# Kernel tuning notes

Hardware: AMD Instinct MI355X
Metric: run time of the kernel (lower is better)

The kernel has to match this reference:

```python
import jax, jax.numpy as jnp
import numpy as np

B, S, H, NH = 4, 2048, 1024, 16
D = H // NH  # head width = 64
SCALE = 1.0 / np.sqrt(np.float32(H))  # NOTE: module scales by rsqrt(hidden_size), not head_width
EPS = 1e-5


def setup_inputs() -> dict:
    key = jax.random.key(0)
    ks = jax.random.split(key, 12)
    def lin(k):
        kw, kb = jax.random.split(k)
        return (jax.random.normal(kw, (H, H), jnp.float32) * 0.02,
                jax.random.normal(kb, (H,), jnp.float32) * 0.02)
    Wq, bq = lin(ks[0]); Wk, bk = lin(ks[1]); Wv, bv = lin(ks[2]); Wm, bm = lin(ks[3])
    q = jax.random.normal(ks[4], (B, S, H), jnp.float32)
    k = jax.random.normal(ks[5], (B, S, H), jnp.float32)
    v = jax.random.normal(ks[6], (B, S, H), jnp.float32)
    # causal mask: True positions are masked with -inf (matches masked_fill semantics)
    mask = jnp.broadcast_to(jnp.triu(jnp.ones((S, S), bool), k=1), (B, S, S))
    gamma = jnp.ones((H,), jnp.float32)
    beta = jnp.zeros((H,), jnp.float32)
    return {"q": q, "k": k, "v": v, "mask": mask,
            "Wq": Wq, "bq": bq, "Wk": Wk, "bk": bk, "Wv": Wv, "bv": bv,
            "Wm": Wm, "bm": bm, "gamma": gamma, "beta": beta}


def layer_norm(x, gamma, beta):
    mu = jnp.mean(x, axis=-1, keepdims=True)
    var = jnp.mean(jnp.square(x - mu), axis=-1, keepdims=True)
    return (x - mu) * jax.lax.rsqrt(var + EPS) * gamma + beta


def reference(q, k, v, mask, Wq, bq, Wk, bk, Wv, bv, Wm, bm, gamma, beta):
    residual = q
    # projections, split into heads: [B, NH, S, D]
    qh = (q @ Wq.T + bq).reshape(B, S, NH, D).transpose(0, 2, 1, 3)
    kh = (k @ Wk.T + bk).reshape(B, S, NH, D).transpose(0, 2, 1, 3)
    vh = (v @ Wv.T + bv).reshape(B, S, NH, D).transpose(0, 2, 1, 3)
    scores = jnp.einsum('bhsd,bhtd->bhst', qh, kh) * SCALE
    scores = jnp.where(mask[:, None, :, :], -jnp.inf, scores)
    attn = jax.nn.softmax(scores, axis=-1)  # dropout is identity (p=0 / eval)
    ctx = jnp.einsum('bhst,bhtd->bhsd', attn, vh)
    ctx = ctx.transpose(0, 2, 1, 3).reshape(B, S, H)
    out = ctx @ Wm.T + bm
    out = layer_norm(out + residual, gamma, beta)
    return out, attn
```

## Files before the change

kernel.cpp:

```cpp
#include <hip/hip_runtime.h>
#include <hip/hip_bf16.h>

#define S_LEN   2048
#define NHEAD   16
#define HID     1024
#define HDIM    64
#define ATT_SCALE 0.03125f
#define LN_EPS  1e-5f
#define EXP_C1  0.04508422002778011f
#define EXP_C2  (-11.541560327111707f)

using bf16x8 = __attribute__((ext_vector_type(8))) short;
using f32x4  = __attribute__((ext_vector_type(4))) float;
typedef unsigned short u16;

__device__ __forceinline__ u16 f2b(float f) {
  union { float f; unsigned u; } v; v.f = f;
  unsigned r = v.u + 0x7fffu + ((v.u >> 16) & 1u);
  return (u16)(r >> 16);
}

__device__ __forceinline__ float fexp2(float x) {
  return __builtin_amdgcn_exp2f(x);
}

__device__ __forceinline__ unsigned cvtpk(float a, float b) {
  unsigned r;
  asm("v_cvt_pk_bf16_f32 %0, %1, %2" : "=v"(r) : "v"(a), "v"(b));
  return r;
}

__device__ __forceinline__ f32x4 mfma16(bf16x8 a, bf16x8 b, f32x4 c) {
  return __builtin_amdgcn_mfma_f32_16x16x32_bf16(a, b, c, 0, 0, 0);
}

__device__ __forceinline__ void gld_lds16(const u16* g, void* l) {
  __builtin_amdgcn_global_load_lds(
      (const __attribute__((address_space(1))) void*)g,
      (__attribute__((address_space(3))) void*)l, 16, 0, 0);
}

__global__ __launch_bounds__(256) void cvt_w4(
    const float* __restrict__ s0, const float* __restrict__ s1,
    const float* __restrict__ s2, const float* __restrict__ s3,
    u16* __restrict__ d0, u16* __restrict__ d1,
    u16* __restrict__ d2, u16* __restrict__ d3)
{
  int i = blockIdx.x * 256 + threadIdx.x;
  int stride = gridDim.x * 256;
  for (; i < 1048576; i += stride) {
    int seg = i >> 18, off = i & 262143;
    const float* s = seg == 0 ? s0 : seg == 1 ? s1 : seg == 2 ? s2 : s3;
    u16*         d = seg == 0 ? d0 : seg == 1 ? d1 : seg == 2 ? d2 : d3;
    float4 vv = ((const float4*)s)[off];
    ushort4 o;
    o.x = f2b(vv.x); o.y = f2b(vv.y); o.z = f2b(vv.z); o.w = f2b(vv.w);
    ((ushort4*)d)[off] = o;
  }
}

__global__ __launch_bounds__(256) void cvt_x3(
    const float* __restrict__ s0, const float* __restrict__ s1,
    const float* __restrict__ s2,
    u16* __restrict__ d0, u16* __restrict__ d1, u16* __restrict__ d2)
{
  int i = blockIdx.x * 256 + threadIdx.x;
  int stride = gridDim.x * 256;
  for (; i < 6291456; i += stride) {
    int seg = i >> 21, off = i & 2097151;
    const float* s = seg == 0 ? s0 : seg == 1 ? s1 : s2;
    u16*         d = seg == 0 ? d0 : seg == 1 ? d1 : d2;
    float4 vv = ((const float4*)s)[off];
    ushort4 o;
    o.x = f2b(vv.x); o.y = f2b(vv.y); o.z = f2b(vv.z); o.w = f2b(vv.w);
    ((ushort4*)d)[off] = o;
  }
}

__global__ __launch_bounds__(256) void qkv_gemm(
    const u16* __restrict__ xq, const u16* __restrict__ xk,
    const u16* __restrict__ xv,
    const u16* __restrict__ Wq, const u16* __restrict__ Wk,
    const u16* __restrict__ Wv,
    const float* __restrict__ bq, const float* __restrict__ bk,
    const float* __restrict__ bv,
    u16* __restrict__ qo, u16* __restrict__ ko, u16* __restrict__ vo,
    float* __restrict__ fill)
{
  const int t = threadIdx.x;

  if (blockIdx.y >= 192) {
    int u = ((int)blockIdx.y - 192) * 8 + (int)blockIdx.x;
    int bh = u & 63, tmp = u >> 6, qtb = tmp >> 3, rg = tmp & 7;
    int w4 = (15 - qtb) * 32;
    f32x4* base = (f32x4*)(fill + ((long)bh * 2048 + qtb * 128 + rg * 16) * 2048
                                + (qtb + 1) * 128);
    f32x4 z = { 0.f, 0.f, 0.f, 0.f };
    for (int r = 0; r < 16; ++r) {
      f32x4* rp = base + (long)r * 512;
      for (int cc = t; cc < w4; cc += 256) rp[cc] = z;
    }
    return;
  }

  const int yg = blockIdx.y;
  const int op = yg >> 6;
  const u16*   A    = op == 0 ? xq : op == 1 ? xk : xv;
  const u16*   W    = op == 0 ? Wq : op == 1 ? Wk : Wv;
  const float* bias = op == 0 ? bq : op == 1 ? bk : bv;
  u16*         out  = op == 0 ? qo : op == 1 ? ko : vo;

  __shared__ __align__(16) u16 As[128 * 64];
  __shared__ __align__(16) u16 Bs[128 * 64];
  const int m0 = (yg & 63) * 128, n0 = blockIdx.x * 128;
  const int w = t >> 6, lane = t & 63, g = lane >> 4, c = lane & 15;
  const int wr = w >> 1, wc = w & 1;

  f32x4 acc[4][4] = {};

  for (int k0 = 0; k0 < 1024; k0 += 64) {
    __syncthreads();
#pragma unroll
    for (int it = 0; it < 4; ++it) {
      int chunk = it * 256 + t;
      int row = chunk >> 3, cf = (chunk & 7) * 8;
      gld_lds16(&A[(long)(m0 + row) * 1024 + k0 + cf], &As[(it * 256 + (t & ~63)) * 8]);
      gld_lds16(&W[(long)(n0 + row) * 1024 + k0 + cf], &Bs[(it * 256 + (t & ~63)) * 8]);
    }
    __syncthreads();
#pragma unroll
    for (int kk = 0; kk < 2; ++kk) {
      bf16x8 am[4], bn[4];
#pragma unroll
      for (int m = 0; m < 4; ++m)
        am[m] = *(const bf16x8*)(&As[(wr * 64 + m * 16 + c) * 64 + kk * 32 + g * 8]);
#pragma unroll
      for (int n = 0; n < 4; ++n)
        bn[n] = *(const bf16x8*)(&Bs[(wc * 64 + n * 16 + c) * 64 + kk * 32 + g * 8]);
#pragma unroll
      for (int m = 0; m < 4; ++m)
#pragma unroll
        for (int n = 0; n < 4; ++n)
          acc[m][n] = mfma16(am[m], bn[n], acc[m][n]);
    }
  }

#pragma unroll
  for (int m = 0; m < 4; ++m)
#pragma unroll
    for (int n = 0; n < 4; ++n)
#pragma unroll
      for (int r = 0; r < 4; ++r) {
        int grow = m0 + wr * 64 + m * 16 + g * 4 + r;
        int gcol = n0 + wc * 64 + n * 16 + c;
        float v = acc[m][n][r] + bias[gcol];
        int b = grow >> 11, s = grow & 2047;
        int h = gcol >> 6, d = gcol & 63;
        out[(((long)(b * 16 + h) * 2048 + s) << 6) + d] = f2b(v);
      }
}

__global__ __launch_bounds__(256) void gemm_out(
    const u16* __restrict__ A, const u16* __restrict__ W,
    float* __restrict__ out_f)
{
  __shared__ __align__(16) u16 As[128 * 64];
  __shared__ __align__(16) u16 Bs[128 * 64];
  const int t = threadIdx.x;
  const int m0 = blockIdx.y * 128, n0 = blockIdx.x * 128;
  const int w = t >> 6, lane = t & 63, g = lane >> 4, c = lane & 15;
  const int wr = w >> 1, wc = w & 1;

  f32x4 acc[4][4] = {};

  for (int k0 = 0; k0 < 1024; k0 += 64) {
    __syncthreads();
#pragma unroll
    for (int it = 0; it < 4; ++it) {
      int chunk = it * 256 + t;
      int row = chunk >> 3, cf = (chunk & 7) * 8;
      gld_lds16(&A[(long)(m0 + row) * 1024 + k0 + cf], &As[(it * 256 + (t & ~63)) * 8]);
      gld_lds16(&W[(long)(n0 + row) * 1024 + k0 + cf], &Bs[(it * 256 + (t & ~63)) * 8]);
    }
    __syncthreads();
#pragma unroll
    for (int kk = 0; kk < 2; ++kk) {
      bf16x8 am[4], bn[4];
#pragma unroll
      for (int m = 0; m < 4; ++m)
        am[m] = *(const bf16x8*)(&As[(wr * 64 + m * 16 + c) * 64 + kk * 32 + g * 8]);
#pragma unroll
      for (int n = 0; n < 4; ++n)
        bn[n] = *(const bf16x8*)(&Bs[(wc * 64 + n * 16 + c) * 64 + kk * 32 + g * 8]);
#pragma unroll
      for (int m = 0; m < 4; ++m)
#pragma unroll
        for (int n = 0; n < 4; ++n)
          acc[m][n] = mfma16(am[m], bn[n], acc[m][n]);
    }
  }

#pragma unroll
  for (int m = 0; m < 4; ++m)
#pragma unroll
    for (int n = 0; n < 4; ++n)
#pragma unroll
      for (int r = 0; r < 4; ++r) {
        int grow = m0 + wr * 64 + m * 16 + g * 4 + r;
        int gcol = n0 + wc * 64 + n * 16 + c;
        out_f[(long)grow * 1024 + gcol] = acc[m][n][r];
      }
}

__global__ __launch_bounds__(256) void transpose_v(const u16* __restrict__ vh,
                                                   u16* __restrict__ vt) {
  __shared__ __align__(16) u16 tile[64 * 72];
  const int t = threadIdx.x;
  const u16* src = vh + ((long)blockIdx.y * 2048 + blockIdx.x * 64) * 64;
#pragma unroll
  for (int it = 0; it < 2; ++it) {
    int chunk = it * 256 + t;
    int s = chunk >> 3, d0 = (chunk & 7) * 8;
    *(int4*)(&tile[s * 72 + d0]) = *(const int4*)(&src[s * 64 + d0]);
  }
  __syncthreads();
  u16* dst = vt + (long)blockIdx.y * 64 * 2048 + blockIdx.x * 64;
#pragma unroll
  for (int it = 0; it < 2; ++it) {
    int chunk = it * 256 + t;
    int d = chunk >> 3, s0 = (chunk & 7) * 8;
    __attribute__((ext_vector_type(8))) unsigned short v;
#pragma unroll
    for (int x = 0; x < 8; ++x) v[x] = tile[(s0 + x) * 72 + d];
    *(decltype(v)*)(&dst[(long)d * 2048 + s0]) = v;
  }
}

__global__ __launch_bounds__(512, 4) void attn_kernel(
    const u16* __restrict__ qh, const u16* __restrict__ kh,
    const u16* __restrict__ vt, u16* __restrict__ ctx,
    float* __restrict__ attn)
{
  __shared__ __align__(16) char lds[49152];
  const int t = threadIdx.x, w = t >> 6, lane = t & 63, g = lane >> 4, c = lane & 15;
  const int n = blockIdx.x;
  const int bh = (n & 7) * 8 + ((n >> 3) & 7);
  const int qtb = 15 - (n >> 6);
  const int q0 = qtb * 128;
  const int ktmax = qtb * 2 + 1;
  const long kvbase = (long)bh * 2048 * 64;

  bf16x8 qa[2];
  {
    const u16* qp = qh + kvbase + (long)(q0 + w * 16 + c) * 64 + g * 8;
    qa[0] = *(const bf16x8*)(qp);
    qa[1] = *(const bf16x8*)(qp + 32);
  }
  const int qpos = q0 + w * 16 + c;

  const int srow = t >> 3, sc8 = t & 7;
  const int ksoff = srow * 64 + ((sc8 ^ (srow & 7)) * 8);
  const u16* kbase = kh + kvbase;
  const u16* vbase = vt + (long)(bh * 64 + srow) * 2048 + ((sc8 ^ (srow & 7)) * 8);

  float lsum = 0.f;
  {
    gld_lds16(kbase + ksoff, lds + w * 1024);
    gld_lds16(kbase + 4096 + ksoff, lds + 8192 + w * 1024);
    for (int p = 0; p <= qtb; ++p) {
      const int kb = (p & 1) * 16384;
      if (p < qtb) {
        const int nb = ((p + 1) & 1) * 16384;
        gld_lds16(kbase + (long)(p + 1) * 8192 + ksoff, lds + nb + w * 1024);
        gld_lds16(kbase + (long)(p + 1) * 8192 + 4096 + ksoff, lds + nb + 8192 + w * 1024);
        asm volatile("s_waitcnt vmcnt(2)" ::: "memory");
      } else {
        asm volatile("s_waitcnt vmcnt(0)" ::: "memory");
      }
      __builtin_amdgcn_sched_barrier(0);
      __builtin_amdgcn_s_barrier();
      __builtin_amdgcn_sched_barrier(0);
      f32x4 sacc[8] = {};
      __builtin_amdgcn_s_setprio(1);
#pragma unroll
      for (int sub = 0; sub < 8; ++sub) {
        int row = sub * 16 + c;
#pragma unroll
        for (int kk = 0; kk < 2; ++kk) {
          bf16x8 av = *(const bf16x8*)(lds + kb + row * 128 + (((kk * 4 + g) ^ (c & 7)) << 4));
          sacc[sub] = mfma16(av, qa[kk], sacc[sub]);
        }
      }
      __builtin_amdgcn_s_setprio(0);
#pragma unroll
      for (int sub = 0; sub < 8; ++sub)
#pragma unroll
        for (int r = 0; r < 4; ++r) {
          int kpos = p * 128 + sub * 16 + g * 4 + r;
          float e = fexp2(fmaf(sacc[sub][r], EXP_C1, EXP_C2));
          lsum += (kpos > qpos) ? 0.f : e;
        }
      __builtin_amdgcn_sched_barrier(0);
      __builtin_amdgcn_s_barrier();
    }
  }
  lsum += __shfl_xor(lsum, 16, 64);
  lsum += __shfl_xor(lsum, 32, 64);
  const float ri = 1.f / lsum;

  char* const Ps = lds + 32768 + w * 2048;
  f32x4 oacc[4] = {};
  gld_lds16(kbase + ksoff, lds + w * 1024);
  gld_lds16(vbase, lds + 16384 + w * 1024);
  for (int kt = 0; kt <= ktmax; ++kt) {
    const int kb = (kt & 1) * 8192;
    if (kt < ktmax) {
      const int nb = ((kt + 1) & 1) * 8192;
      gld_lds16(kbase + (long)(kt + 1) * 4096 + ksoff, lds + nb + w * 1024);
      gld_lds16(vbase + (kt + 1) * 64, lds + 16384 + nb + w * 1024);
      if (kt == 0) { asm volatile("s_waitcnt vmcnt(2)" ::: "memory"); }
      else         { asm volatile("s_waitcnt vmcnt(6)" ::: "memory"); }
    } else {
      asm volatile("s_waitcnt vmcnt(4)" ::: "memory");
    }
    __builtin_amdgcn_sched_barrier(0);
    __builtin_amdgcn_s_barrier();
    __builtin_amdgcn_sched_barrier(0);
    f32x4 sacc[4] = {};
    __builtin_amdgcn_s_setprio(1);
#pragma unroll
    for (int sub = 0; sub < 4; ++sub) {
      int row = sub * 16 + c;
#pragma unroll
      for (int kk = 0; kk < 2; ++kk) {
        bf16x8 av = *(const bf16x8*)(lds + kb + row * 128 + (((kk * 4 + g) ^ (c & 7)) << 4));
        sacc[sub] = mfma16(av, qa[kk], sacc[sub]);
      }
    }
    __builtin_amdgcn_s_setprio(0);
#pragma unroll
    for (int sub = 0; sub < 4; ++sub) {
      float p[4];
#pragma unroll
      for (int r = 0; r < 4; ++r) {
        int kpos = kt * 64 + sub * 16 + g * 4 + r;
        float e = fexp2(fmaf(sacc[sub][r], EXP_C1, EXP_C2)) * ri;
        p[r] = (kpos > qpos) ? 0.f : e;
      }
      uint2 pk = { cvtpk(p[0], p[1]), cvtpk(p[2], p[3]) };
      int chunk = sub * 2 + (g >> 1);
      *(uint2*)(Ps + c * 128 + ((chunk ^ (c & 7)) << 4) + (g & 1) * 8) = pk;
    }
    {
      float* arow0 = attn + ((long)bh * 2048 + q0 + w * 16) * 2048 + kt * 64;
#pragma unroll
      for (int j = 0; j < 4; ++j) {
        int row = j * 4 + g;
        uint2 u = *(const uint2*)(Ps + row * 128 + (((c >> 1) ^ (row & 7)) << 4) + (c & 1) * 8);
        f32x4 pv;
        pv[0] = __uint_as_float((u.x & 0xffffu) << 16);
        pv[1] = __uint_as_float(u.x & 0xffff0000u);
        pv[2] = __uint_as_float((u.y & 0xffffu) << 16);
        pv[3] = __uint_as_float(u.y & 0xffff0000u);
        *(f32x4*)(arow0 + (long)row * 2048 + c * 4) = pv;
      }
    }
    __builtin_amdgcn_s_setprio(1);
#pragma unroll
    for (int kk = 0; kk < 2; ++kk) {
      bf16x8 pa = *(const bf16x8*)(Ps + c * 128 + (((kk * 4 + g) ^ (c & 7)) << 4));
#pragma unroll
      for (int db = 0; db < 4; ++db) {
        bf16x8 vb = *(const bf16x8*)(lds + 16384 + kb + (db * 16 + c) * 128 + (((kk * 4 + g) ^ (c & 7)) << 4));
        oacc[db] = mfma16(pa, vb, oacc[db]);
      }
    }
    __builtin_amdgcn_s_setprio(0);
    __builtin_amdgcn_sched_barrier(0);
    __builtin_amdgcn_s_barrier();
  }

  {
    int b = bh >> 4, h = bh & 15;
#pragma unroll
    for (int db = 0; db < 4; ++db)
#pragma unroll
      for (int r = 0; r < 4; ++r) {
        int s = q0 + w * 16 + g * 4 + r;
        ctx[(long)(b * 2048 + s) * 1024 + h * 64 + db * 16 + c] = f2b(oacc[db][r]);
      }
  }
}

__global__ __launch_bounds__(256) void ln_kernel(
    const float* __restrict__ y, const float* __restrict__ bm,
    const float* __restrict__ resid, const float* __restrict__ gamma,
    const float* __restrict__ beta, float* __restrict__ out)
{
  __shared__ float red[8];
  const long row = blockIdx.x;
  const int t = threadIdx.x, w = t >> 6, lane = t & 63;
  const float4* yp = (const float4*)(y + row * 1024);
  const float4* rp = (const float4*)(resid + row * 1024);
  float4 x = yp[t], rv = rp[t], bv = ((const float4*)bm)[t];
  x.x += rv.x + bv.x; x.y += rv.y + bv.y; x.z += rv.z + bv.z; x.w += rv.w + bv.w;

  float s1 = x.x + x.y + x.z + x.w;
#pragma unroll
  for (int o = 32; o; o >>= 1) s1 += __shfl_xor(s1, o, 64);
  if (!lane) red[w] = s1;
  __syncthreads();
  float mean = (red[0] + red[1] + red[2] + red[3]) * (1.f / 1024.f);

  float dx = x.x - mean, dy = x.y - mean, dz = x.z - mean, dw = x.w - mean;
  float s2 = dx * dx + dy * dy + dz * dz + dw * dw;
#pragma unroll
  for (int o = 32; o; o >>= 1) s2 += __shfl_xor(s2, o, 64);
  if (!lane) red[4 + w] = s2;
  __syncthreads();
  float var = (red[4] + red[5] + red[6] + red[7]) * (1.f / 1024.f);
  float rs = rsqrtf(var + LN_EPS);

  float4 gv = ((const float4*)gamma)[t], be = ((const float4*)beta)[t];
  float4 o4;
  o4.x = dx * rs * gv.x + be.x;
  o4.y = dy * rs * gv.y + be.y;
  o4.z = dz * rs * gv.z + be.z;
  o4.w = dw * rs * gv.w + be.w;
  ((float4*)(out + row * 1024))[t] = o4;
}

extern "C" void kernel_launch(void* const* d_in, const int* in_sizes, int n_in,
                              void* d_out, int out_size, void* d_ws, size_t ws_size,
                              hipStream_t stream) {
  const float* q     = (const float*)d_in[0];
  const float* k     = (const float*)d_in[1];
  const float* v     = (const float*)d_in[2];
  const float* Wq    = (const float*)d_in[4];
  const float* bq    = (const float*)d_in[5];
  const float* Wk    = (const float*)d_in[6];
  const float* bk    = (const float*)d_in[7];
  const float* Wv    = (const float*)d_in[8];
  const float* bv    = (const float*)d_in[9];
  const float* Wm    = (const float*)d_in[10];
  const float* bm    = (const float*)d_in[11];
  const float* gamma = (const float*)d_in[12];
  const float* beta  = (const float*)d_in[13];

  float* out  = (float*)d_out;
  float* attn = out + 8388608;

  char* ws = (char*)d_ws;
  u16* qh   = (u16*)(ws);
  u16* kh   = (u16*)(ws + 16777216);
  u16* vh   = (u16*)(ws + 33554432);
  u16* ctx  = (u16*)(ws + 33554432);
  u16* Wqb  = (u16*)(ws + 50331648);
  u16* Wkb  = Wqb + 1048576;
  u16* Wvb  = Wkb + 1048576;
  u16* Wmb  = Wvb + 1048576;
  u16* xq   = (u16*)(ws + 58720256);
  u16* vt   = (u16*)(ws + 58720256);
  u16* xk   = (u16*)(ws + 75497472);
  u16* xv   = (u16*)(ws + 92274688);
  float* y  = (float*)(ws + 75497472);

  dim3 blk(256);

  cvt_w4<<<1024, blk, 0, stream>>>(Wq, Wk, Wv, Wm, Wqb, Wkb, Wvb, Wmb);
  cvt_x3<<<2048, blk, 0, stream>>>(q, k, v, xq, xk, xv);

  qkv_gemm<<<dim3(8, 1152), blk, 0, stream>>>(
      xq, xk, xv, Wqb, Wkb, Wvb, bq, bk, bv, qh, kh, vh, attn);

  transpose_v<<<dim3(32, 64), blk, 0, stream>>>(vh, vt);

  attn_kernel<<<1024, 512, 0, stream>>>(qh, kh, vt, ctx, attn);

  gemm_out<<<dim3(8, 64), blk, 0, stream>>>(ctx, Wmb, y);

  ln_kernel<<<8192, blk, 0, stream>>>(y, bm, q, gamma, beta, out);
}
```

Baseline: 465.1 us.

## Double per-block query tile to 256 rows with triple-buffered K/V loads

Each attention block now handles 256 query rows (two 16-row groups per wave) instead of 128, so every K/V tile loaded into LDS is reused across twice as many queries and the grid halves to 512 blocks. K/V staging moves from double to triple buffering with adjusted vmcnt waits, and the per-iteration end barrier is removed. Block ordering is changed so the heavy and light causal tiles are interleaved for load balance. The cost is more LDS (64KB) and registers per block, which lowers occupancy and leaves fewer blocks to spread across CUs. Dropping the trailing barrier depends on the third buffer to keep the reused Ps and K/V regions free of read/write races.

```diff
diff --git a/kernel.cpp b/kernel.cpp
--- a/kernel.cpp
+++ b/kernel.cpp
@@ -241,38 +241,44 @@
     const u16* __restrict__ vt, u16* __restrict__ ctx,
     float* __restrict__ attn)
 {
-  __shared__ __align__(16) char lds[49152];
+  __shared__ __align__(16) char lds[65536];
   const int t = threadIdx.x, w = t >> 6, lane = t & 63, g = lane >> 4, c = lane & 15;
   const int n = blockIdx.x;
+  const int qtb = (n < 256) ? 7 - (n >> 6) : ((n - 256) >> 6);
   const int bh = (n & 7) * 8 + ((n >> 3) & 7);
-  const int qtb = 15 - (n >> 6);
-  const int q0 = qtb * 128;
-  const int ktmax = qtb * 2 + 1;
+  const int q0 = qtb * 256;
+  const int pmax  = qtb * 2 + 1;
+  const int ktmax = qtb * 4 + 3;
   const long kvbase = (long)bh * 2048 * 64;
 
-  bf16x8 qa[2];
+  bf16x8 qa[2][2];
+  int qpos[2];
+#pragma unroll
+  for (int h = 0; h < 2; ++h) {
+    const u16* qp = qh + kvbase + (long)(q0 + w * 32 + h * 16 + c) * 64 + g * 8;
+    qa[h][0] = *(const bf16x8*)(qp);
+    qa[h][1] = *(const bf16x8*)(qp + 32);
+    qpos[h] = q0 + w * 32 + h * 16 + c;
+  }
+
+  const int srow = t >> 3, sc8 = t & 7;
+  const int scol = (sc8 ^ (srow & 7)) * 8;
+  const u16* kbase = kh + kvbase;
+  const u16* vbase = vt + (long)(bh * 64 + srow) * 2048 + scol;
+
+  float lsum[2] = { 0.f, 0.f };
   {
-    const u16* qp = qh + kvbase + (long)(q0 + w * 16 + c) * 64 + g * 8;
-    qa[0] = *(const bf16x8*)(qp);
-    qa[1] = *(const bf16x8*)(qp + 32);
-  }
-  const int qpos = q0 + w * 16 + c;
-
-  const int srow = t >> 3, sc8 = t & 7;
-  const int ksoff = srow * 64 + ((sc8 ^ (srow & 7)) * 8);
-  const u16* kbase = kh + kvbase;
-  const u16* vbase = vt + (long)(bh * 64 + srow) * 2048 + ((sc8 ^ (srow & 7)) * 8);
-
-  float lsum = 0.f;
-  {
-    gld_lds16(kbase + ksoff, lds + w * 1024);
-    gld_lds16(kbase + 4096 + ksoff, lds + 8192 + w * 1024);
-    for (int p = 0; p <= qtb; ++p) {
-      const int kb = (p & 1) * 16384;
-      if (p < qtb) {
-        const int nb = ((p + 1) & 1) * 16384;
-        gld_lds16(kbase + (long)(p + 1) * 8192 + ksoff, lds + nb + w * 1024);
-        gld_lds16(kbase + (long)(p + 1) * 8192 + 4096 + ksoff, lds + nb + 8192 + w * 1024);
+#pragma unroll
+    for (int j = 0; j < 2; ++j)
+      gld_lds16(kbase + (j * 64 + srow) * 64 + scol, lds + j * 8192 + w * 1024);
+    for (int p = 0; p <= pmax; ++p) {
+      const int cur = (p % 3) * 16384;
+      if (p < pmax) {
+        const int nb = ((p + 1) % 3) * 16384;
+#pragma unroll
+        for (int j = 0; j < 2; ++j)
+          gld_lds16(kbase + ((long)(p + 1) * 128 + j * 64 + srow) * 64 + scol,
+                    lds + nb + j * 8192 + w * 1024);
         asm volatile("s_waitcnt vmcnt(2)" ::: "memory");
       } else {
         asm volatile("s_waitcnt vmcnt(0)" ::: "memory");
@@ -280,115 +286,126 @@
       __builtin_amdgcn_sched_barrier(0);
       __builtin_amdgcn_s_barrier();
       __builtin_amdgcn_sched_barrier(0);
-      f32x4 sacc[8] = {};
-      __builtin_amdgcn_s_setprio(1);
-#pragma unroll
-      for (int sub = 0; sub < 8; ++sub) {
-        int row = sub * 16 + c;
-#pragma unroll
-        for (int kk = 0; kk < 2; ++kk) {
-          bf16x8 av = *(const bf16x8*)(lds + kb + row * 128 + (((kk * 4 + g) ^ (c & 7)) << 4));
-          sacc[sub] = mfma16(av, qa[kk], sacc[sub]);
+#pragma unroll
+      for (int h = 0; h < 2; ++h) {
+        f32x4 sacc[8] = {};
+        __builtin_amdgcn_s_setprio(1);
+#pragma unroll
+        for (int sub = 0; sub < 8; ++sub) {
+          int row = sub * 16 + c;
+#pragma unroll
+          for (int kk = 0; kk < 2; ++kk) {
+            bf16x8 av = *(const bf16x8*)(lds + cur + row * 128 + (((kk * 4 + g) ^ (c & 7)) << 4));
+            sacc[sub] = mfma16(av, qa[h][kk], sacc[sub]);
+          }
         }
-      }
-      __builtin_amdgcn_s_setprio(0);
-#pragma unroll
-      for (int sub = 0; sub < 8; ++sub)
-#pragma unroll
-        for (int r = 0; r < 4; ++r) {
-          int kpos = p * 128 + sub * 16 + g * 4 + r;
-          float e = fexp2(fmaf(sacc[sub][r], EXP_C1, EXP_C2));
-          lsum += (kpos > qpos) ? 0.f : e;
-        }
-      __builtin_amdgcn_sched_barrier(0);
-      __builtin_amdgcn_s_barrier();
-    }
-  }
-  lsum += __shfl_xor(lsum, 16, 64);
-  lsum += __shfl_xor(lsum, 32, 64);
-  const float ri = 1.f / lsum;
-
-  char* const Ps = lds + 32768 + w * 2048;
-  f32x4 oacc[4] = {};
-  gld_lds16(kbase + ksoff, lds + w * 1024);
-  gld_lds16(vbase, lds + 16384 + w * 1024);
+        __builtin_amdgcn_s_setprio(0);
+#pragma unroll
+        for (int sub = 0; sub < 8; ++sub)
+#pragma unroll
+          for (int r = 0; r < 4; ++r) {
+            int kpos = p * 128 + sub * 16 + g * 4 + r;
+            float e = fexp2(fmaf(sacc[sub][r], EXP_C1, EXP_C2));
+            lsum[h] += (kpos > qpos[h]) ? 0.f : e;
+          }
+      }
+    }
+  }
+  float ri[2];
+#pragma unroll
+  for (int h = 0; h < 2; ++h) {
+    lsum[h] += __shfl_xor(lsum[h], 16, 64);
+    lsum[h] += __shfl_xor(lsum[h], 32, 64);
+    ri[h] = 1.f / lsum[h];
+  }
+  __builtin_amdgcn_sched_barrier(0);
+  __builtin_amdgcn_s_barrier();
+  __builtin_amdgcn_sched_barrier(0);
+
+  char* const Ps = lds + 49152 + w * 2048;
+  f32x4 oacc[2][4] = {};
+  gld_lds16(kbase + srow * 64 + scol, lds + w * 1024);
+  gld_lds16(vbase, lds + 24576 + w * 1024);
   for (int kt = 0; kt <= ktmax; ++kt) {
-    const int kb = (kt & 1) * 8192;
+    const int cur = (kt % 3) * 8192;
     if (kt < ktmax) {
-      const int nb = ((kt + 1) & 1) * 8192;
-      gld_lds16(kbase + (long)(kt + 1) * 4096 + ksoff, lds + nb + w * 1024);
-      gld_lds16(vbase + (kt + 1) * 64, lds + 16384 + nb + w * 1024);
+      const int nb = ((kt + 1) % 3) * 8192;
+      gld_lds16(kbase + (long)(kt + 1) * 4096 + srow * 64 + scol, lds + nb + w * 1024);
+      gld_lds16(vbase + (kt + 1) * 64, lds + 24576 + nb + w * 1024);
       if (kt == 0) { asm volatile("s_waitcnt vmcnt(2)" ::: "memory"); }
-      else         { asm volatile("s_waitcnt vmcnt(6)" ::: "memory"); }
+      else         { asm volatile("s_waitcnt vmcnt(10)" ::: "memory"); }
     } else {
-      asm volatile("s_waitcnt vmcnt(4)" ::: "memory");
+      asm volatile("s_waitcnt vmcnt(8)" ::: "memory");
     }
     __builtin_amdgcn_sched_barrier(0);
     __builtin_amdgcn_s_barrier();
     __builtin_amdgcn_sched_barrier(0);
-    f32x4 sacc[4] = {};
-    __builtin_amdgcn_s_setprio(1);
-#pragma unroll
-    for (int sub = 0; sub < 4; ++sub) {
-      int row = sub * 16 + c;
+#pragma unroll
+    for (int h = 0; h < 2; ++h) {
+      f32x4 sacc[4] = {};
+      __builtin_amdgcn_s_setprio(1);
+#pragma unroll
+      for (int sub = 0; sub < 4; ++sub) {
+        int row = sub * 16 + c;
+#pragma unroll
+        for (int kk = 0; kk < 2; ++kk) {
+          bf16x8 av = *(const bf16x8*)(lds + cur + row * 128 + (((kk * 4 + g) ^ (c & 7)) << 4));
+          sacc[sub] = mfma16(av, qa[h][kk], sacc[sub]);
+        }
+      }
+      __builtin_amdgcn_s_setprio(0);
+#pragma unroll
+      for (int sub = 0; sub < 4; ++sub) {
+        float p[4];
+#pragma unroll
+        for (int r = 0; r < 4; ++r) {
+          int kpos = kt * 64 + sub * 16 + g * 4 + r;
+          float e = fexp2(fmaf(sacc[sub][r], EXP_C1, EXP_C2)) * ri[h];
+          p[r] = (kpos > qpos[h]) ? 0.f : e;
+        }
+        uint2 pk = { cvtpk(p[0], p[1]), cvtpk(p[2], p[3]) };
+        int chunk = sub * 2 + (g >> 1);
+        *(uint2*)(Ps + c * 128 + ((chunk ^ (c & 7)) << 4) + (g & 1) * 8) = pk;
+      }
+      {
+        float* arow0 = attn + ((long)bh * 2048 + q0 + w * 32 + h * 16) * 2048 + kt * 64;
+#pragma unroll
+        for (int j = 0; j < 4; ++j) {
+          int row = j * 4 + g;
+          uint2 u = *(const uint2*)(Ps + row * 128 + (((c >> 1) ^ (row & 7)) << 4) + (c & 1) * 8);
+          f32x4 pv;
+          pv[0] = __uint_as_float((u.x & 0xffffu) << 16);
+          pv[1] = __uint_as_float(u.x & 0xffff0000u);
+          pv[2] = __uint_as_float((u.y & 0xffffu) << 16);
+          pv[3] = __uint_as_float(u.y & 0xffff0000u);
+          *(f32x4*)(arow0 + (long)row * 2048 + c * 4) = pv;
+        }
+      }
+      __builtin_amdgcn_s_setprio(1);
 #pragma unroll
       for (int kk = 0; kk < 2; ++kk) {
-        bf16x8 av = *(const bf16x8*)(lds + kb + row * 128 + (((kk * 4 + g) ^ (c & 7)) << 4));
-        sacc[sub] = mfma16(av, qa[kk], sacc[sub]);
-      }
-    }
-    __builtin_amdgcn_s_setprio(0);
-#pragma unroll
-    for (int sub = 0; sub < 4; ++sub) {
-      float p[4];
-#pragma unroll
-      for (int r = 0; r < 4; ++r) {
-        int kpos = kt * 64 + sub * 16 + g * 4 + r;
-        float e = fexp2(fmaf(sacc[sub][r], EXP_C1, EXP_C2)) * ri;
-        p[r] = (kpos > qpos) ? 0.f : e;
-      }
-      uint2 pk = { cvtpk(p[0], p[1]), cvtpk(p[2], p[3]) };
-      int chunk = sub * 2 + (g >> 1);
-      *(uint2*)(Ps + c * 128 + ((chunk ^ (c & 7)) << 4) + (g & 1) * 8) = pk;
-    }
-    {
-      float* arow0 = attn + ((long)bh * 2048 + q0 + w * 16) * 2048 + kt * 64;
-#pragma unroll
-      for (int j = 0; j < 4; ++j) {
-        int row = j * 4 + g;
-        uint2 u = *(const uint2*)(Ps + row * 128 + (((c >> 1) ^ (row & 7)) << 4) + (c & 1) * 8);
-        f32x4 pv;
-        pv[0] = __uint_as_float((u.x & 0xffffu) << 16);
-        pv[1] = __uint_as_float(u.x & 0xffff0000u);
-        pv[2] = __uint_as_float((u.y & 0xffffu) << 16);
-        pv[3] = __uint_as_float(u.y & 0xffff0000u);
-        *(f32x4*)(arow0 + (long)row * 2048 + c * 4) = pv;
-      }
-    }
-    __builtin_amdgcn_s_setprio(1);
-#pragma unroll
-    for (int kk = 0; kk < 2; ++kk) {
-      bf16x8 pa = *(const bf16x8*)(Ps + c * 128 + (((kk * 4 + g) ^ (c & 7)) << 4));
-#pragma unroll
-      for (int db = 0; db < 4; ++db) {
-        bf16x8 vb = *(const bf16x8*)(lds + 16384 + kb + (db * 16 + c) * 128 + (((kk * 4 + g) ^ (c & 7)) << 4));
-        oacc[db] = mfma16(pa, vb, oacc[db]);
-      }
-    }
-    __builtin_amdgcn_s_setprio(0);
-    __builtin_amdgcn_sched_barrier(0);
-    __builtin_amdgcn_s_barrier();
+        bf16x8 pa = *(const bf16x8*)(Ps + c * 128 + (((kk * 4 + g) ^ (c & 7)) << 4));
+#pragma unroll
+        for (int db = 0; db < 4; ++db) {
+          bf16x8 vb = *(const bf16x8*)(lds + 24576 + cur + (db * 16 + c) * 128 + (((kk * 4 + g) ^ (c & 7)) << 4));
+          oacc[h][db] = mfma16(pa, vb, oacc[h][db]);
+        }
+      }
+      __builtin_amdgcn_s_setprio(0);
+    }
   }
 
   {
-    int b = bh >> 4, h = bh & 15;
-#pragma unroll
-    for (int db = 0; db < 4; ++db)
-#pragma unroll
-      for (int r = 0; r < 4; ++r) {
-        int s = q0 + w * 16 + g * 4 + r;
-        ctx[(long)(b * 2048 + s) * 1024 + h * 64 + db * 16 + c] = f2b(oacc[db][r]);
-      }
+    int b = bh >> 4, hh = bh & 15;
+#pragma unroll
+    for (int h = 0; h < 2; ++h)
+#pragma unroll
+      for (int db = 0; db < 4; ++db)
+#pragma unroll
+        for (int r = 0; r < 4; ++r) {
+          int s = q0 + w * 32 + h * 16 + g * 4 + r;
+          ctx[(long)(b * 2048 + s) * 1024 + hh * 64 + db * 16 + c] = f2b(oacc[h][db][r]);
+        }
   }
 }
 
@@ -475,7 +492,7 @@
 
   transpose_v<<<dim3(32, 64), blk, 0, stream>>>(vh, vt);
 
-  attn_kernel<<<1024, 512, 0, stream>>>(qh, kh, vt, ctx, attn);
+  attn_kernel<<<512, 512, 0, stream>>>(qh, kh, vt, ctx, attn);
 
   gemm_out<<<dim3(8, 64), blk, 0, stream>>>(ctx, Wmb, y);
 
```

After: 474.2 us. Within noise of the previous version (+2.0%).

## Fuse V transpose into QKV GEMM epilogue and vectorize stores via LDS staging

Applied to the files above, without the earlier changes.

The QKV GEMM epilogue now stages the bf16 output tile in shared memory and writes Q/K with 16-byte vector stores. V is written already transposed into the vt layout, so the separate transpose_v kernel and its extra read and write of V are gone. The attention kernel's ctx write is also staged through LDS so it can use vectorized row stores. The workspace layout is reshuffled to fit. This costs extra LDS traffic, barriers and a larger shared allocation in the GEMM, and the strided LDS column reads for the V transpose may hit bank conflicts.

```diff
diff --git a/kernel.cpp b/kernel.cpp
--- a/kernel.cpp
+++ b/kernel.cpp
@@ -11,6 +11,7 @@
 #define EXP_C2  (-11.541560327111707f)
 
 using bf16x8 = __attribute__((ext_vector_type(8))) short;
+using u16x8  = __attribute__((ext_vector_type(8))) unsigned short;
 using f32x4  = __attribute__((ext_vector_type(4))) float;
 typedef unsigned short u16;
 
@@ -84,7 +85,7 @@
     const u16* __restrict__ Wv,
     const float* __restrict__ bq, const float* __restrict__ bk,
     const float* __restrict__ bv,
-    u16* __restrict__ qo, u16* __restrict__ ko, u16* __restrict__ vo,
+    u16* __restrict__ qo, u16* __restrict__ ko, u16* __restrict__ vt,
     float* __restrict__ fill)
 {
   const int t = threadIdx.x;
@@ -108,10 +109,10 @@
   const u16*   A    = op == 0 ? xq : op == 1 ? xk : xv;
   const u16*   W    = op == 0 ? Wq : op == 1 ? Wk : Wv;
   const float* bias = op == 0 ? bq : op == 1 ? bk : bv;
-  u16*         out  = op == 0 ? qo : op == 1 ? ko : vo;
-
-  __shared__ __align__(16) u16 As[128 * 64];
-  __shared__ __align__(16) u16 Bs[128 * 64];
+
+  __shared__ __align__(16) char smem[34816];
+  u16* As = (u16*)smem;
+  u16* Bs = (u16*)(smem + 16384);
   const int m0 = (yg & 63) * 128, n0 = blockIdx.x * 128;
   const int w = t >> 6, lane = t & 63, g = lane >> 4, c = lane & 15;
   const int wr = w >> 1, wc = w & 1;
@@ -145,19 +146,45 @@
     }
   }
 
+  __syncthreads();
+  u16* Cl = (u16*)smem;
 #pragma unroll
   for (int m = 0; m < 4; ++m)
 #pragma unroll
     for (int n = 0; n < 4; ++n)
 #pragma unroll
       for (int r = 0; r < 4; ++r) {
-        int grow = m0 + wr * 64 + m * 16 + g * 4 + r;
-        int gcol = n0 + wc * 64 + n * 16 + c;
-        float v = acc[m][n][r] + bias[gcol];
-        int b = grow >> 11, s = grow & 2047;
-        int h = gcol >> 6, d = gcol & 63;
-        out[(((long)(b * 16 + h) * 2048 + s) << 6) + d] = f2b(v);
-      }
+        int row = wr * 64 + m * 16 + g * 4 + r;
+        int col = wc * 64 + n * 16 + c;
+        Cl[row * 136 + col] = f2b(acc[m][n][r] + bias[n0 + col]);
+      }
+  __syncthreads();
+
+  if (op < 2) {
+    u16* out = op == 0 ? qo : ko;
+#pragma unroll
+    for (int pass = 0; pass < 8; ++pass) {
+      int unit = pass * 32 + (t >> 3), c8 = t & 7;
+      int row = unit >> 1, half = unit & 1;
+      int grow = m0 + row;
+      int b = grow >> 11, s = grow & 2047, h = (n0 + half * 64) >> 6;
+      u16x8 vv = *(const u16x8*)(Cl + row * 136 + half * 64 + c8 * 8);
+      *(u16x8*)(out + (((long)(b * 16 + h) * 2048 + s) << 6) + c8 * 8) = vv;
+    }
+  } else {
+    int b = m0 >> 11, sbase = m0 & 2047;
+#pragma unroll
+    for (int pass = 0; pass < 8; ++pass) {
+      int unit = pass * 32 + (t >> 3), c8 = t & 7;
+      int colL = unit >> 1, chunk = unit & 1;
+      int h = (n0 + colL) >> 6, d = (n0 + colL) & 63;
+      int sl = chunk * 64 + c8 * 8;
+      u16x8 vv;
+#pragma unroll
+      for (int i = 0; i < 8; ++i) vv[i] = Cl[(sl + i) * 136 + colL];
+      *(u16x8*)(vt + (long)((b * 16 + h) * 64 + d) * 2048 + sbase + sl) = vv;
+    }
+  }
 }
 
 __global__ __launch_bounds__(256) void gemm_out(
@@ -210,30 +237,6 @@
         int gcol = n0 + wc * 64 + n * 16 + c;
         out_f[(long)grow * 1024 + gcol] = acc[m][n][r];
       }
-}
-
-__global__ __launch_bounds__(256) void transpose_v(const u16* __restrict__ vh,
-                                                   u16* __restrict__ vt) {
-  __shared__ __align__(16) u16 tile[64 * 72];
-  const int t = threadIdx.x;
-  const u16* src = vh + ((long)blockIdx.y * 2048 + blockIdx.x * 64) * 64;
-#pragma unroll
-  for (int it = 0; it < 2; ++it) {
-    int chunk = it * 256 + t;
-    int s = chunk >> 3, d0 = (chunk & 7) * 8;
-    *(int4*)(&tile[s * 72 + d0]) = *(const int4*)(&src[s * 64 + d0]);
-  }
-  __syncthreads();
-  u16* dst = vt + (long)blockIdx.y * 64 * 2048 + blockIdx.x * 64;
-#pragma unroll
-  for (int it = 0; it < 2; ++it) {
-    int chunk = it * 256 + t;
-    int d = chunk >> 3, s0 = (chunk & 7) * 8;
-    __attribute__((ext_vector_type(8))) unsigned short v;
-#pragma unroll
-    for (int x = 0; x < 8; ++x) v[x] = tile[(s0 + x) * 72 + d];
-    *(decltype(v)*)(&dst[(long)d * 2048 + s0]) = v;
-  }
 }
 
 __global__ __launch_bounds__(512, 4) void attn_kernel(
@@ -380,15 +383,23 @@
     __builtin_amdgcn_s_barrier();
   }
 
+  __builtin_amdgcn_sched_barrier(0);
+  __builtin_amdgcn_s_barrier();
+  __builtin_amdgcn_sched_barrier(0);
   {
-    int b = bh >> 4, h = bh & 15;
+    u16* Cl = (u16*)(lds + w * 4352);
 #pragma unroll
     for (int db = 0; db < 4; ++db)
 #pragma unroll
-      for (int r = 0; r < 4; ++r) {
-        int s = q0 + w * 16 + g * 4 + r;
-        ctx[(long)(b * 2048 + s) * 1024 + h * 64 + db * 16 + c] = f2b(oacc[db][r]);
-      }
+      for (int r = 0; r < 4; ++r)
+        Cl[(g * 4 + r) * 136 + db * 16 + c] = f2b(oacc[db][r]);
+    int b = bh >> 4, hh = bh & 15;
+#pragma unroll
+    for (int pass = 0; pass < 2; ++pass) {
+      int row16 = pass * 8 + (lane >> 3), c8 = lane & 7;
+      u16x8 vv = *(const u16x8*)(Cl + row16 * 136 + c8 * 8);
+      *(u16x8*)(ctx + (long)(b * 2048 + q0 + w * 16 + row16) * 1024 + hh * 64 + c8 * 8) = vv;
+    }
   }
 }
 
@@ -453,17 +464,16 @@
   char* ws = (char*)d_ws;
   u16* qh   = (u16*)(ws);
   u16* kh   = (u16*)(ws + 16777216);
-  u16* vh   = (u16*)(ws + 33554432);
-  u16* ctx  = (u16*)(ws + 33554432);
-  u16* Wqb  = (u16*)(ws + 50331648);
+  u16* vt   = (u16*)(ws + 33554432);
+  u16* xq   = (u16*)(ws + 50331648);
+  u16* ctx  = (u16*)(ws + 50331648);
+  u16* xk   = (u16*)(ws + 67108864);
+  u16* xv   = (u16*)(ws + 83886080);
+  float* y  = (float*)(ws + 67108864);
+  u16* Wqb  = (u16*)(ws + 100663296);
   u16* Wkb  = Wqb + 1048576;
   u16* Wvb  = Wkb + 1048576;
   u16* Wmb  = Wvb + 1048576;
-  u16* xq   = (u16*)(ws + 58720256);
-  u16* vt   = (u16*)(ws + 58720256);
-  u16* xk   = (u16*)(ws + 75497472);
-  u16* xv   = (u16*)(ws + 92274688);
-  float* y  = (float*)(ws + 75497472);
 
   dim3 blk(256);
 
@@ -471,9 +481,7 @@
   cvt_x3<<<2048, blk, 0, stream>>>(q, k, v, xq, xk, xv);
 
   qkv_gemm<<<dim3(8, 1152), blk, 0, stream>>>(
-      xq, xk, xv, Wqb, Wkb, Wvb, bq, bk, bv, qh, kh, vh, attn);
-
-  transpose_v<<<dim3(32, 64), blk, 0, stream>>>(vh, vt);
+      xq, xk, xv, Wqb, Wkb, Wvb, bq, bk, bv, qh, kh, vt, attn);
 
   attn_kernel<<<1024, 512, 0, stream>>>(qh, kh, vt, ctx, attn);
 
```

Measured after the change: 463.3 us. Within noise of the previous version (-0.4%).
